# Kernel tuning notes

Measured on AMD Instinct MI355X. Metric: run time of the kernel, lower is better.

## Reference

```python
import jax, jax.numpy as jnp
import numpy as np
from jax import lax

KH, KW, PAD = 3, 3, 1  # kernel_size and paddings from init_kwargs


def _sign_pm1(v):
    # tf.sign with zeros mapped to -1
    return jnp.where(v > 0, jnp.float32(1.0), jnp.float32(-1.0)).astype(v.dtype)


def setup_inputs() -> dict:
    key = jax.random.key(0)
    k1, k2, k3 = jax.random.split(key, 3)
    x = jax.random.normal(k1, (32, 56, 56, 256), dtype=jnp.float32)
    kernel = jax.random.normal(k2, (KH, KW, 256, 256), dtype=jnp.float32) * 0.05
    bias = jax.random.normal(k3, (256,), dtype=jnp.float32) * 0.01
    return {"x": x, "kernel": kernel, "bias": bias}


def reference(x, kernel, bias):
    # pad input spatially (NHWC)
    xp = jnp.pad(x, ((0, 0), (PAD, PAD), (PAD, PAD), (0, 0)))

    # binarize kernel: static batch dim known -> alpha = mean(|W|) over (kh, kw, cin)
    bin_k = _sign_pm1(kernel)
    alpha = jnp.mean(jnp.abs(kernel), axis=(0, 1, 2))  # (Cout,)

    # binarize input: batch dim dynamic in TF -> beta = mean(|x|) over channels, keepdims
    bin_x = _sign_pm1(xp)                               # (N, H+2P, W+2P, C)
    beta = jnp.mean(jnp.abs(xp), axis=3, keepdims=True)  # (N, H+2P, W+2P, 1)

    # K = avg_pool(beta, kernel window, stride 1, VALID)
    K = lax.reduce_window(beta, jnp.float32(0.0), lax.add,
                          (1, KH, KW, 1), (1, 1, 1, 1), 'VALID') / (KH * KW)
    Ka = K * alpha  # (N, H, W, Cout) via broadcast

    conv = lax.conv_general_dilated(
        bin_x, bin_k, window_strides=(1, 1), padding='VALID',
        dimension_numbers=('NHWC', 'HWIO', 'NHWC'))  # (N, H, W, Cout)

    return conv * Ka + bias
```

## Files before the change

kernel.cpp:

```cpp
#include <hip/hip_runtime.h>
#include <cstdint>
#include <cstddef>

#define N_ 32
#define H_ 56
#define W_ 56
#define C_ 256
#define HP 58
#define WP 58

typedef int v4i  __attribute__((ext_vector_type(4)));
typedef int v16i __attribute__((ext_vector_type(16)));

__global__ __launch_bounds__(256) void pack_w(const float* __restrict__ k,
                                              signed char* __restrict__ wi8,
                                              float* __restrict__ palpha) {
    int idx = blockIdx.x;
    int p = idx >> 2, q = idx & 3;
    int co = threadIdx.x;
    float s = 0.f;
    #pragma unroll
    for (int half = 0; half < 2; ++half) {
        int kc = q * 2 + half;
        unsigned wrd[8];
        #pragma unroll
        for (int e = 0; e < 8; ++e) {
            unsigned wv = 0;
            #pragma unroll
            for (int j = 0; j < 4; ++j) {
                float v = k[(size_t)(p * 256 + kc * 32 + e * 4 + j) * 256 + co];
                s += fabsf(v);
                wv |= ((v > 0.f) ? 0x01u : 0xFFu) << (8 * j);
            }
            wrd[e] = wv;
        }
        v4i lo = {(int)wrd[0], (int)wrd[1], (int)wrd[2], (int)wrd[3]};
        v4i hi = {(int)wrd[4], (int)wrd[5], (int)wrd[6], (int)wrd[7]};
        size_t base = ((size_t)(p * 8 + kc) * 256 + co) * 2;
        ((v4i*)wi8)[base]     = lo;
        ((v4i*)wi8)[base + 1] = hi;
    }
    palpha[idx * 256 + co] = s;
}

__global__ __launch_bounds__(256) void pack_x(const float4* __restrict__ x4,
                                              signed char* __restrict__ xi8,
                                              float* __restrict__ beta) {
    int bi = blockIdx.x;
    int n = bi / HP, y = bi % HP;
    int wave = threadIdx.x >> 6, lane = threadIdx.x & 63;
    for (int xc = wave; xc < WP; xc += 4) {
        bool inb = (y >= 1 && y <= H_ && xc >= 1 && xc <= W_);
        float4 v = make_float4(0.f, 0.f, 0.f, 0.f);
        if (inb)
            v = x4[(((size_t)n * H_ + (y - 1)) * W_ + (xc - 1)) * 64 + lane];
        unsigned w = ((v.x > 0.f) ? 0x01u : 0xFFu)
                   | (((v.y > 0.f) ? 0x01u : 0xFFu) << 8)
                   | (((v.z > 0.f) ? 0x01u : 0xFFu) << 16)
                   | (((v.w > 0.f) ? 0x01u : 0xFFu) << 24);
        float s = fabsf(v.x) + fabsf(v.y) + fabsf(v.z) + fabsf(v.w);
        #pragma unroll
        for (int m = 32; m >= 1; m >>= 1) s += __shfl_xor(s, m, 64);
        size_t pix = (size_t)bi * WP + xc;
        ((unsigned*)xi8)[pix * 64 + lane] = w;
        if (lane == 0) beta[pix] = s * (1.f / 256.f);
    }
}

__device__ __forceinline__ void epilogue(const v16i& acc, int mb, int svar,
                                         const float* bS, float alpha, float bv,
                                         int co, size_t obase,
                                         float* __restrict__ out) {
    #pragma unroll
    for (int r = 0; r < 16; ++r) {
        int row = (r & 3) + 8 * (r >> 2) + 4 * svar;
        int m = mb + row;
        if (m < 112) {
            int hl = (m >= 56);
            int w = m - 56 * hl;
            float val = (float)acc[r] * (bS[m] * alpha) + bv;
            out[obase + ((size_t)hl * W_ + w) * C_ + co] = val;
        }
    }
}

__global__ __launch_bounds__(512, 4) void bconv(
        const signed char* __restrict__ xi8, const float* __restrict__ beta,
        const signed char* __restrict__ wi8, const float* __restrict__ palpha,
        const float* __restrict__ bias, float* __restrict__ out) {
    int bid = blockIdx.x;
    int bi = (bid & 7) * 112 + (bid >> 3);
    int n = bi / 28;
    int hb = (bi - n * 28) * 2;

    int tid = threadIdx.x;
    int lane = tid & 63, wid = tid >> 6;
    int wm = wid >> 2, wn = wid & 3;
    int l31 = lane & 31, svar = lane >> 5;

    __shared__ __align__(16) signed char xs[4 * WP * 256];
    __shared__ float brow[4 * WP];
    __shared__ float bS[112];

    {
        const v4i* src = (const v4i*)(xi8 + (size_t)(n * HP + hb) * WP * 256);
        v4i* dst = (v4i*)xs;
        for (int s = tid; s < 4 * WP * 16; s += 512) {
            int pp = s >> 4, sl = s & 15;
            dst[(pp << 4) | (sl ^ (pp & 15))] = src[s];
        }
        const float* bsrc = beta + (size_t)(n * HP + hb) * WP;
        for (int i = tid; i < 4 * WP; i += 512) brow[i] = bsrc[i];
    }
    __syncthreads();

    if (tid < 112) {
        int r = (tid >= 56);
        int w = tid - 56 * r;
        float s = 0.f;
        #pragma unroll
        for (int rr = 0; rr < 3; ++rr)
            #pragma unroll
            for (int d = 0; d < 3; ++d) s += brow[(r + rr) * WP + w + d];
        bS[tid] = s * (1.f / 9.f);
    }

    int m0 = wm * 64 + l31;
    int m1 = m0 + 32;
    int m1e = m1 < 112 ? m1 : 111;
    int hl0 = (m0 >= 56), hl1 = (m1e >= 56);
    int pb0 = hl0 * WP + (m0 - 56 * hl0);
    int pb1 = hl1 * WP + (m1e - 56 * hl1);

    int co0 = wn * 64 + l31, co1 = co0 + 32;
    int vb0 = co0 * 2 + svar, vb1 = vb0 + 64;

    v16i acc00 = {0,0,0,0,0,0,0,0,0,0,0,0,0,0,0,0};
    v16i acc01 = acc00, acc10 = acc00, acc11 = acc00;

    const v4i* xsv = (const v4i*)xs;
    const v4i* wv  = (const v4i*)wi8;

    for (int tap = 0; tap < 9; ++tap) {
        int kh = (tap * 11) >> 5;
        int kw = tap - kh * 3;
        int p0 = pb0 + kh * WP + kw;
        int p1 = pb1 + kh * WP + kw;
        int a0 = p0 << 4, x0 = p0 & 15;
        int a1 = p1 << 4, x1 = p1 & 15;
        const v4i* bq = wv + (size_t)tap * 8 * 512;
        #pragma unroll
        for (int kc = 0; kc < 8; ++kc) {
            int sl = kc * 2 + svar;
            v4i A0 = xsv[a0 | (sl ^ x0)];
            v4i A1 = xsv[a1 | (sl ^ x1)];
            v4i B0 = bq[vb0];
            v4i B1 = bq[vb1];
            acc00 = __builtin_amdgcn_mfma_i32_32x32x32_i8(A0, B0, acc00, 0, 0, 0);
            acc01 = __builtin_amdgcn_mfma_i32_32x32x32_i8(A0, B1, acc01, 0, 0, 0);
            acc10 = __builtin_amdgcn_mfma_i32_32x32x32_i8(A1, B0, acc10, 0, 0, 0);
            acc11 = __builtin_amdgcn_mfma_i32_32x32x32_i8(A1, B1, acc11, 0, 0, 0);
            bq += 512;
        }
    }

    __syncthreads();

    float a0s = 0.f, a1s = 0.f;
    for (int i = 0; i < 36; ++i) {
        a0s += palpha[i * 256 + co0];
        a1s += palpha[i * 256 + co1];
    }
    a0s *= (1.f / 2304.f);
    a1s *= (1.f / 2304.f);
    float bv0 = bias[co0], bv1 = bias[co1];

    size_t obase = (size_t)(n * H_ + hb) * W_ * C_;
    epilogue(acc00, wm * 64,      svar, bS, a0s, bv0, co0, obase, out);
    epilogue(acc01, wm * 64,      svar, bS, a1s, bv1, co1, obase, out);
    epilogue(acc10, wm * 64 + 32, svar, bS, a0s, bv0, co0, obase, out);
    epilogue(acc11, wm * 64 + 32, svar, bS, a1s, bv1, co1, obase, out);
}

extern "C" void kernel_launch(void* const* d_in, const int* in_sizes, int n_in,
                              void* d_out, int out_size, void* d_ws, size_t ws_size,
                              hipStream_t stream) {
    const float* x    = (const float*)d_in[0];
    const float* k    = (const float*)d_in[1];
    const float* bias = (const float*)d_in[2];
    float* out = (float*)d_out;

    char* ws = (char*)d_ws;
    signed char* wi8    = (signed char*)(ws);
    float*       palpha = (float*)(ws + 589824);
    signed char* xi8    = (signed char*)(ws + 626688);
    float*       beta   = (float*)(ws + 28184576);

    pack_w<<<36, 256, 0, stream>>>(k, wi8, palpha);
    pack_x<<<N_ * HP, 256, 0, stream>>>((const float4*)x, xi8, beta);
    bconv<<<896, 512, 0, stream>>>(xi8, beta, wi8, palpha, bias, out);
}
```

Before: 293.3 us.

## Fuse input binarization into conv kernel and software-pipeline MFMA operand loads

Drops the separate pack_x kernel. Each conv block now reads the fp32 input rows it needs, binarizes them and computes per-pixel channel means directly into shared memory, which avoids the int8 workspace round trip and one launch. Each 2-row block reads 4 padded rows, so about twice as much fp32 input is read in total because of the halo. The inner loop also prefetches the next A/B operands from LDS and global memory while the current MFMAs issue, which costs extra registers.

```diff
diff --git a/kernel.cpp b/kernel.cpp
--- a/kernel.cpp
+++ b/kernel.cpp
@@ -43,30 +43,6 @@
     palpha[idx * 256 + co] = s;
 }
 
-__global__ __launch_bounds__(256) void pack_x(const float4* __restrict__ x4,
-                                              signed char* __restrict__ xi8,
-                                              float* __restrict__ beta) {
-    int bi = blockIdx.x;
-    int n = bi / HP, y = bi % HP;
-    int wave = threadIdx.x >> 6, lane = threadIdx.x & 63;
-    for (int xc = wave; xc < WP; xc += 4) {
-        bool inb = (y >= 1 && y <= H_ && xc >= 1 && xc <= W_);
-        float4 v = make_float4(0.f, 0.f, 0.f, 0.f);
-        if (inb)
-            v = x4[(((size_t)n * H_ + (y - 1)) * W_ + (xc - 1)) * 64 + lane];
-        unsigned w = ((v.x > 0.f) ? 0x01u : 0xFFu)
-                   | (((v.y > 0.f) ? 0x01u : 0xFFu) << 8)
-                   | (((v.z > 0.f) ? 0x01u : 0xFFu) << 16)
-                   | (((v.w > 0.f) ? 0x01u : 0xFFu) << 24);
-        float s = fabsf(v.x) + fabsf(v.y) + fabsf(v.z) + fabsf(v.w);
-        #pragma unroll
-        for (int m = 32; m >= 1; m >>= 1) s += __shfl_xor(s, m, 64);
-        size_t pix = (size_t)bi * WP + xc;
-        ((unsigned*)xi8)[pix * 64 + lane] = w;
-        if (lane == 0) beta[pix] = s * (1.f / 256.f);
-    }
-}
-
 __device__ __forceinline__ void epilogue(const v16i& acc, int mb, int svar,
                                          const float* bS, float alpha, float bv,
                                          int co, size_t obase,
@@ -85,7 +61,7 @@
 }
 
 __global__ __launch_bounds__(512, 4) void bconv(
-        const signed char* __restrict__ xi8, const float* __restrict__ beta,
+        const float4* __restrict__ x4,
         const signed char* __restrict__ wi8, const float* __restrict__ palpha,
         const float* __restrict__ bias, float* __restrict__ out) {
     int bid = blockIdx.x;
@@ -103,14 +79,26 @@
     __shared__ float bS[112];
 
     {
-        const v4i* src = (const v4i*)(xi8 + (size_t)(n * HP + hb) * WP * 256);
-        v4i* dst = (v4i*)xs;
-        for (int s = tid; s < 4 * WP * 16; s += 512) {
-            int pp = s >> 4, sl = s & 15;
-            dst[(pp << 4) | (sl ^ (pp & 15))] = src[s];
-        }
-        const float* bsrc = beta + (size_t)(n * HP + hb) * WP;
-        for (int i = tid; i < 4 * WP; i += 512) brow[i] = bsrc[i];
+        int sl4 = lane >> 2;
+        int bo  = (lane & 3) << 2;
+        for (int i = 0; i < 29; ++i) {
+            int pp = wid + 8 * i;
+            int r = pp / WP, xc = pp - r * WP;
+            int ypad = hb + r;
+            bool inb = (ypad >= 1 && ypad <= H_ && xc >= 1 && xc <= W_);
+            float4 v = make_float4(0.f, 0.f, 0.f, 0.f);
+            if (inb)
+                v = x4[(((size_t)n * H_ + (ypad - 1)) * W_ + (xc - 1)) * 64 + lane];
+            unsigned wb = ((v.x > 0.f) ? 0x01u : 0xFFu)
+                        | (((v.y > 0.f) ? 0x01u : 0xFFu) << 8)
+                        | (((v.z > 0.f) ? 0x01u : 0xFFu) << 16)
+                        | (((v.w > 0.f) ? 0x01u : 0xFFu) << 24);
+            *(unsigned*)&xs[pp * 256 + ((sl4 ^ (pp & 15)) << 4) + bo] = wb;
+            float s = fabsf(v.x) + fabsf(v.y) + fabsf(v.z) + fabsf(v.w);
+            #pragma unroll
+            for (int m = 32; m >= 1; m >>= 1) s += __shfl_xor(s, m, 64);
+            if (lane == 0) brow[pp] = s * (1.f / 256.f);
+        }
     }
     __syncthreads();
 
@@ -141,27 +129,41 @@
     const v4i* xsv = (const v4i*)xs;
     const v4i* wv  = (const v4i*)wi8;
 
+    int a0c = pb0 << 4, x0c = pb0 & 15;
+    int a1c = pb1 << 4, x1c = pb1 & 15;
+    const v4i* bqc = wv;
+
+    v4i A0 = xsv[a0c | (svar ^ x0c)];
+    v4i A1 = xsv[a1c | (svar ^ x1c)];
+    v4i B0 = bqc[vb0];
+    v4i B1 = bqc[vb1];
+
     for (int tap = 0; tap < 9; ++tap) {
-        int kh = (tap * 11) >> 5;
-        int kw = tap - kh * 3;
-        int p0 = pb0 + kh * WP + kw;
-        int p1 = pb1 + kh * WP + kw;
-        int a0 = p0 << 4, x0 = p0 & 15;
-        int a1 = p1 << 4, x1 = p1 & 15;
-        const v4i* bq = wv + (size_t)tap * 8 * 512;
+        int tn = (tap < 8) ? tap + 1 : 8;
+        int khn = (tn * 11) >> 5, kwn = tn - khn * 3;
+        int p0n = pb0 + khn * WP + kwn, p1n = pb1 + khn * WP + kwn;
+        int a0n = p0n << 4, x0n = p0n & 15;
+        int a1n = p1n << 4, x1n = p1n & 15;
+        const v4i* bqn = wv + (size_t)tn * 4096;
         #pragma unroll
         for (int kc = 0; kc < 8; ++kc) {
-            int sl = kc * 2 + svar;
-            v4i A0 = xsv[a0 | (sl ^ x0)];
-            v4i A1 = xsv[a1 | (sl ^ x1)];
-            v4i B0 = bq[vb0];
-            v4i B1 = bq[vb1];
+            const int nkc = (kc == 7) ? 0 : kc + 1;
+            const int sln = nkc * 2 + svar;
+            int A0a, A1a;
+            const v4i* bq2;
+            if (kc == 7) { A0a = a0n | (sln ^ x0n); A1a = a1n | (sln ^ x1n); bq2 = bqn; }
+            else         { A0a = a0c | (sln ^ x0c); A1a = a1c | (sln ^ x1c); bq2 = bqc; }
+            v4i A0n_ = xsv[A0a];
+            v4i A1n_ = xsv[A1a];
+            v4i B0n_ = bq2[nkc * 512 + vb0];
+            v4i B1n_ = bq2[nkc * 512 + vb1];
             acc00 = __builtin_amdgcn_mfma_i32_32x32x32_i8(A0, B0, acc00, 0, 0, 0);
             acc01 = __builtin_amdgcn_mfma_i32_32x32x32_i8(A0, B1, acc01, 0, 0, 0);
             acc10 = __builtin_amdgcn_mfma_i32_32x32x32_i8(A1, B0, acc10, 0, 0, 0);
             acc11 = __builtin_amdgcn_mfma_i32_32x32x32_i8(A1, B1, acc11, 0, 0, 0);
-            bq += 512;
-        }
+            A0 = A0n_; A1 = A1n_; B0 = B0n_; B1 = B1n_;
+        }
+        a0c = a0n; x0c = x0n; a1c = a1n; x1c = x1n; bqc = bqn;
     }
 
     __syncthreads();
@@ -193,10 +195,7 @@
     char* ws = (char*)d_ws;
     signed char* wi8    = (signed char*)(ws);
     float*       palpha = (float*)(ws + 589824);
-    signed char* xi8    = (signed char*)(ws + 626688);
-    float*       beta   = (float*)(ws + 28184576);
 
     pack_w<<<36, 256, 0, stream>>>(k, wi8, palpha);
-    pack_x<<<N_ * HP, 256, 0, stream>>>((const float4*)x, xi8, beta);
-    bconv<<<896, 512, 0, stream>>>(xi8, beta, wi8, palpha, bias, out);
-}
+    bconv<<<896, 512, 0, stream>>>((const float4*)x, wi8, palpha, bias, out);
+}
```

After: 260.0 us. 1.13x faster.
